# Optimization experiments

Measured on AMD Instinct MI355X. Metric: run time of the kernel, lower is better.

Reference implementation:

```python
import jax, jax.numpy as jnp
import numpy as np

H, L, N = 512, 2048, 64  # channels, seq len, SSM state size


def _make_dplr_hippo(n):
    # make_HiPPO / make_NPLR_HiPPO / make_DPLR_HiPPO from the source
    p0 = np.sqrt(1.0 + 2.0 * np.arange(n))
    A = p0[:, None] * p0[None, :]
    A = np.tril(A) - np.diag(np.arange(n))
    nhippo = -A
    P = np.sqrt(np.arange(n) + 0.5)
    B = np.sqrt(2.0 * np.arange(n) + 1.0)
    S = nhippo + P[:, None] * P[None, :]
    S_diag = np.diagonal(S)
    Lam_re = np.mean(S_diag) * np.ones_like(S_diag)
    Lam_im, V = jnp.linalg.eigh(jnp.asarray(S, jnp.complex64) * (-1j))
    Pc = V.conj().T @ jnp.asarray(P, jnp.complex64)
    Bc = V.conj().T @ jnp.asarray(B, jnp.complex64)
    return (jnp.asarray(Lam_re, jnp.float32), jnp.asarray(Lam_im, jnp.float32),
            Pc, Bc)


def setup_inputs() -> dict:
    key = jax.random.key(0)
    k_u, k_c, k_s = jax.random.split(key, 3)
    Lre, Lim, Pc, Bc = _make_dplr_hippo(N)
    tile = lambda v: jnp.tile(v[None, :], (H, 1)).astype(jnp.float32)  # (H,N)
    return {
        "u": jax.random.normal(k_u, (L, H), dtype=jnp.float32),
        "x0_re": jnp.zeros((N, H), jnp.float32),
        "x0_im": jnp.zeros((N, H), jnp.float32),
        "Lambda_re": tile(Lre),
        "Lambda_im": tile(Lim),
        "P_re": tile(Pc.real), "P_im": tile(Pc.imag),
        "B_re": tile(Bc.real), "B_im": tile(Bc.imag),
        "C": jax.random.normal(k_c, (H, N, 2), jnp.float32) * (0.5 ** 0.5),
        "D": jnp.ones((H, 1), jnp.float32),
        "log_step": jax.random.uniform(k_s, (H, 1), jnp.float32,
                                       minval=np.log(1e-3), maxval=np.log(1e-1)),
    }


def _discretize(Lam, P, B, Ct, step):
    # discrete_DPLR with Q = P (as in setup); per-channel, vmapped over H.
    n = Lam.shape[0]
    I = jnp.eye(n, dtype=jnp.complex64)
    A = jnp.diag(Lam) - P[:, None] * P.conj()[None, :]
    A0 = (2.0 / step) * I + A
    Dd = jnp.diag(1.0 / (2.0 / step - Lam))
    Qc = P.conj()[None, :]            # (1,N)
    P2 = P[:, None]                   # (N,1)
    A1 = Dd - (Dd @ P2) * (1.0 / (1.0 + Qc @ Dd @ P2)) * (Qc @ Dd)
    Ab = A1 @ A0                      # (N,N)
    Bb = 2.0 * (A1 @ B[:, None])[:, 0]
    AbL = jnp.linalg.matrix_power(Ab, L)
    Cb = (Ct[None, :] @ jnp.linalg.inv(I - AbL).conj()).conj()[0]
    return Ab, Bb, Cb


def _forward(u, x0_re, x0_im, Lambda_re, Lambda_im, P_re, P_im,
             B_re, B_im, C, D, log_step):
    Lam = jnp.clip(Lambda_re, None, -0.0001) + 1j * Lambda_im  # (H,N)
    Pc = P_re + 1j * P_im
    Bc = B_re + 1j * B_im
    Cc = C[..., 0] + 1j * C[..., 1]
    step = jnp.exp(log_step)[:, 0]                              # (H,)
    Ab, Bb, Cb = jax.vmap(_discretize)(Lam, Pc, Bc, Cc, step)   # (H,N,N),(H,N),(H,N)

    x0 = jnp.transpose(x0_re + 1j * x0_im)                      # (H,N) complex

    def body(x, u_t):  # x: (H,N) complex, u_t: (H,)
        x = jnp.einsum('hnm,hm->hn', Ab, x) + Bb * u_t[:, None]
        y = jnp.einsum('hn,hn->h', Cb, x)
        return x, y.real

    _, ys = jax.lax.scan(body, x0, u)                           # ys: (L,H)
    return ys + u * D[:, 0][None, :]                            # (L,H) float32


def reference(u, x0_re, x0_im, Lambda_re, Lambda_im, P_re, P_im,
              B_re, B_im, C, D, log_step):
    return _forward(u, x0_re, x0_im, Lambda_re, Lambda_im, P_re, P_im,
                    B_re, B_im, C, D, log_step)
```

## Files before the change

kernel.cpp:

```cpp
#include <hip/hip_runtime.h>

#define HH 512
#define LL 2048
#define NN 64
#define TT 64
#define CC 32
#define NLDA 68
#define SP 72

typedef __attribute__((ext_vector_type(8))) short bf16x8_t;
typedef __attribute__((ext_vector_type(4))) float floatx4;

__device__ __forceinline__ float2 cmul(float2 a, float2 b) {
    return make_float2(a.x * b.x - a.y * b.y, a.x * b.y + a.y * b.x);
}
__device__ __forceinline__ float2 crecip(float2 a) {
    float id = 1.0f / (a.x * a.x + a.y * a.y);
    return make_float2(a.x * id, -a.y * id);
}
template <int CTRL>
__device__ __forceinline__ float dpp_mov(float x) {
    return __int_as_float(__builtin_amdgcn_update_dpp(
        0, __float_as_int(x), CTRL, 0xf, 0xf, true));
}
__device__ __forceinline__ float wave_sum_bcast(float x) {
    x += dpp_mov<0x111>(x);
    x += dpp_mov<0x112>(x);
    x += dpp_mov<0x114>(x);
    x += dpp_mov<0x118>(x);
    x += dpp_mov<0x142>(x);
    x += dpp_mov<0x143>(x);
    return __int_as_float(__builtin_amdgcn_readlane(__float_as_int(x), 63));
}
__device__ __forceinline__ float rlane(float x, int i) {
    return __int_as_float(__builtin_amdgcn_readlane(__float_as_int(x), i));
}
__device__ __forceinline__ unsigned short f2bf(float f) {
    unsigned int u = __float_as_uint(f);
    u += 0x7FFFu + ((u >> 16) & 1u);
    return (unsigned short)(u >> 16);
}
__device__ __forceinline__ float bf2f(unsigned short s) {
    return __uint_as_float(((unsigned int)s) << 16);
}

__device__ __forceinline__ void closed_form(
    int h, int n,
    const float* __restrict__ Lre, const float* __restrict__ Lim,
    const float* __restrict__ Pre, const float* __restrict__ Pim,
    const float* __restrict__ Bre, const float* __restrict__ Bim,
    const float* __restrict__ logstep,
    float2& da, float2& DPv, float2& tv, float2& bb) {
    float step = expf(logstep[h]);
    float as = 2.0f / step;
    float lr = fminf(Lre[h * NN + n], -1e-4f);
    float li = Lim[h * NN + n];
    float2 a = make_float2(as + lr, li);
    float2 Dn = crecip(make_float2(as - lr, -li));
    float2 P = make_float2(Pre[h * NN + n], Pim[h * NN + n]);
    float2 Bv = make_float2(Bre[h * NN + n], Bim[h * NN + n]);
    float2 cP = make_float2(P.x, -P.y);
    float p2 = P.x * P.x + P.y * P.y;
    float2 rt = cmul(cmul(cP, Dn), Bv);
    float2 e = make_float2(wave_sum_bcast(Dn.x * p2), wave_sum_bcast(Dn.y * p2));
    float2 rv = make_float2(wave_sum_bcast(rt.x), wave_sum_bcast(rt.y));
    float2 cc = crecip(make_float2(1.0f + e.x, e.y));
    da = cmul(Dn, a);
    DPv = cmul(Dn, P);
    float2 tmp = cmul(cc, make_float2(da.x - e.x, da.y - e.y));
    tv = cmul(cP, make_float2(1.0f + tmp.x, tmp.y));
    float2 crv = cmul(cc, rv);
    float2 cd = cmul(crv, DPv);
    float2 db = cmul(Dn, Bv);
    bb = make_float2(2.0f * (db.x - cd.x), 2.0f * (db.y - cd.y));
}

__device__ __forceinline__ void pack_tiles(
    unsigned short* mRh, unsigned short* mRl,
    unsigned short* mIh, unsigned short* mIl,
    unsigned short* mTRh, unsigned short* mTRl,
    unsigned short* mTIh, unsigned short* mTIl,
    int w, int lm, int q, const float Cr[4][4], const float Ci[4][4]) {
    #pragma unroll
    for (int nt = 0; nt < 4; ++nt) {
        const int c = nt * 16 + lm;
        unsigned short hr[4], lr_[4], hi_[4], li_[4];
        #pragma unroll
        for (int reg = 0; reg < 4; ++reg) {
            const float xr = Cr[nt][reg], xi = Ci[nt][reg];
            hr[reg] = f2bf(xr); lr_[reg] = f2bf(xr - bf2f(hr[reg]));
            hi_[reg] = f2bf(xi); li_[reg] = f2bf(xi - bf2f(hi_[reg]));
            const int r = 16 * w + 4 * q + reg;
            const int rm = r * 64 + (c ^ ((r & 7) << 3));
            mRh[rm] = hr[reg]; mRl[rm] = lr_[reg];
            mIh[rm] = hi_[reg]; mIl[rm] = li_[reg];
        }
        const int tb = c * 64 + ((16 * w + 4 * q) ^ ((c & 7) << 3));
        *(ushort4*)&mTRh[tb] = make_ushort4(hr[0], hr[1], hr[2], hr[3]);
        *(ushort4*)&mTRl[tb] = make_ushort4(lr_[0], lr_[1], lr_[2], lr_[3]);
        *(ushort4*)&mTIh[tb] = make_ushort4(hi_[0], hi_[1], hi_[2], hi_[3]);
        *(ushort4*)&mTIl[tb] = make_ushort4(li_[0], li_[1], li_[2], li_[3]);
    }
}

extern "C" __global__ void __launch_bounds__(256, 2)
k_fused(const float* __restrict__ Lre, const float* __restrict__ Lim,
        const float* __restrict__ Pre, const float* __restrict__ Pim,
        const float* __restrict__ Bre, const float* __restrict__ Bim,
        const float* __restrict__ Cmat, const float* __restrict__ logstep,
        const float* __restrict__ u, const float* __restrict__ Dvec,
        const float* __restrict__ x0_re, const float* __restrict__ x0_im,
        float2* __restrict__ wM, float* __restrict__ out) {
    extern __shared__ __align__(16) char smem[];
    const int tid = threadIdx.x;
    const int h = blockIdx.x;

    unsigned short* mRh  = (unsigned short*)smem;
    unsigned short* mRl  = mRh + 4096;
    unsigned short* mIh  = mRl + 4096;
    unsigned short* mIl  = mIh + 4096;
    unsigned short* mTRh = mIl + 4096;
    unsigned short* mTRl = mTRh + 4096;
    unsigned short* mTIh = mTRl + 4096;
    unsigned short* mTIl = mTIh + 4096;
    float* Nr = (float*)smem;
    float* Ni = Nr + 64 * NLDA;
    float2* pp   = (float2*)(smem + 36864);
    float2* sda  = (float2*)(smem + 70016);
    float2* sDP  = (float2*)(smem + 70528);
    float2* st   = (float2*)(smem + 71040);
    float2* sBb  = (float2*)(smem + 71552);
    float2* srhs = (float2*)(smem + 72064);
    float2* sx   = (float2*)(smem + 72576);
    unsigned short* sVr  = (unsigned short*)smem;
    unsigned short* sVi  = (unsigned short*)(smem + 9216);
    unsigned short* sXrh = (unsigned short*)(smem + 18432);
    unsigned short* sXrl = (unsigned short*)(smem + 23040);
    unsigned short* sXih = (unsigned short*)(smem + 27648);
    unsigned short* sXil = (unsigned short*)(smem + 32256);
    float*          su   = (float*)(smem + 36864);
    float*          sK   = (float*)(smem + 45056);
    float*          y0   = (float*)(smem + 45312);
    float2*         sP   = (float2*)(smem + 53632);

    const int w = tid >> 6;
    const int lane = tid & 63;
    const int lm = lane & 15, q = lane >> 4;

    if (tid < NN) {
        float2 da, DPv, tv, bb;
        closed_form(h, tid, Lre, Lim, Pre, Pim, Bre, Bim, logstep,
                    da, DPv, tv, bb);
        sda[tid] = da; sDP[tid] = DPv; st[tid] = tv; sBb[tid] = bb;
        srhs[tid] = make_float2(Cmat[h * NN * 2 + tid * 2],
                                -Cmat[h * NN * 2 + tid * 2 + 1]);
    }
    __syncthreads();

    {
        float Cr[4][4], Ci[4][4];
        #pragma unroll
        for (int nt = 0; nt < 4; ++nt) {
            const int c = nt * 16 + lm;
            const float2 tc = st[c];
            #pragma unroll
            for (int reg = 0; reg < 4; ++reg) {
                const int r = 16 * w + 4 * q + reg;
                const float2 dp = sDP[r];
                float vr = -(dp.x * tc.x - dp.y * tc.y);
                float vi = -(dp.x * tc.y + dp.y * tc.x);
                if (r == c) { vr += sda[r].x; vi += sda[r].y; }
                Cr[nt][reg] = vr; Ci[nt][reg] = vi;
            }
        }
        pack_tiles(mRh, mRl, mIh, mIl, mTRh, mTRl, mTIh, mTIl,
                   w, lm, q, Cr, Ci);
    }
    __syncthreads();

    const int arow = (16 * w + lm) * 64;
    const int asw  = (lm & 7) << 3;
    for (int it = 0; it < 11; ++it) {
        floatx4 z4 = {0.f, 0.f, 0.f, 0.f};
        floatx4 aP[4] = {z4, z4, z4, z4};
        floatx4 aQ[4] = {z4, z4, z4, z4};
        floatx4 aC[4] = {z4, z4, z4, z4};
        for (int k2 = 0; k2 < 2; ++k2) {
            const int ko = (k2 * 32 + q * 8) ^ asw;
            const int ao = arow + ko;
            const bf16x8_t ARh = *(const bf16x8_t*)&mRh[ao];
            const bf16x8_t ARl = *(const bf16x8_t*)&mRl[ao];
            const bf16x8_t AIh = *(const bf16x8_t*)&mIh[ao];
            const bf16x8_t AIl = *(const bf16x8_t*)&mIl[ao];
            bf16x8_t BRh[4], BRl[4], BIh[4], BIl[4];
            #pragma unroll
            for (int nt = 0; nt < 4; ++nt) {
                const int bo = (nt * 16 + lm) * 64 + ko;
                BRh[nt] = *(const bf16x8_t*)&mTRh[bo];
                BRl[nt] = *(const bf16x8_t*)&mTRl[bo];
                BIh[nt] = *(const bf16x8_t*)&mTIh[bo];
                BIl[nt] = *(const bf16x8_t*)&mTIl[bo];
            }
            #pragma unroll
            for (int nt = 0; nt < 4; ++nt) {
                aP[nt] = __builtin_amdgcn_mfma_f32_16x16x32_bf16(ARh, BRh[nt], aP[nt], 0, 0, 0);
                aP[nt] = __builtin_amdgcn_mfma_f32_16x16x32_bf16(ARh, BRl[nt], aP[nt], 0, 0, 0);
                aP[nt] = __builtin_amdgcn_mfma_f32_16x16x32_bf16(ARl, BRh[nt], aP[nt], 0, 0, 0);
                aQ[nt] = __builtin_amdgcn_mfma_f32_16x16x32_bf16(AIh, BIh[nt], aQ[nt], 0, 0, 0);
                aQ[nt] = __builtin_amdgcn_mfma_f32_16x16x32_bf16(AIh, BIl[nt], aQ[nt], 0, 0, 0);
                aQ[nt] = __builtin_amdgcn_mfma_f32_16x16x32_bf16(AIl, BIh[nt], aQ[nt], 0, 0, 0);
                aC[nt] = __builtin_amdgcn_mfma_f32_16x16x32_bf16(ARh, BIh[nt], aC[nt], 0, 0, 0);
                aC[nt] = __builtin_amdgcn_mfma_f32_16x16x32_bf16(ARh, BIl[nt], aC[nt], 0, 0, 0);
                aC[nt] = __builtin_amdgcn_mfma_f32_16x16x32_bf16(ARl, BIh[nt], aC[nt], 0, 0, 0);
                aC[nt] = __builtin_amdgcn_mfma_f32_16x16x32_bf16(AIh, BRh[nt], aC[nt], 0, 0, 0);
                aC[nt] = __builtin_amdgcn_mfma_f32_16x16x32_bf16(AIh, BRl[nt], aC[nt], 0, 0, 0);
                aC[nt] = __builtin_amdgcn_mfma_f32_16x16x32_bf16(AIl, BRh[nt], aC[nt], 0, 0, 0);
            }
        }
        __syncthreads();
        if (it < 10) {
            float Cr[4][4], Ci[4][4];
            #pragma unroll
            for (int nt = 0; nt < 4; ++nt)
                #pragma unroll
                for (int reg = 0; reg < 4; ++reg) {
                    Cr[nt][reg] = aP[nt][reg] - aQ[nt][reg];
                    Ci[nt][reg] = aC[nt][reg];
                }
            pack_tiles(mRh, mRl, mIh, mIl, mTRh, mTRl, mTIh, mTIl,
                       w, lm, q, Cr, Ci);
            __syncthreads();
            if (it == 5) {
                for (int idx = tid; idx < NN * NN; idx += 256) {
                    const int c = idx >> 6, k = idx & 63;
                    const int e = c * 64 + (k ^ ((c & 7) << 3));
                    wM[h * NN * NN + idx] = make_float2(
                        bf2f(mTRh[e]) + bf2f(mTRl[e]),
                        bf2f(mTIh[e]) + bf2f(mTIl[e]));
                }
            }
        } else {
            #pragma unroll
            for (int nt = 0; nt < 4; ++nt) {
                const int c = nt * 16 + lm;
                #pragma unroll
                for (int reg = 0; reg < 4; ++reg) {
                    const int r = 16 * w + 4 * q + reg;
                    Nr[r * NLDA + c] = aP[nt][reg] - aQ[nt][reg];
                    Ni[r * NLDA + c] = aC[nt][reg];
                }
            }
            __syncthreads();
        }
    }

    if (tid < NN) sx[tid] = srhs[tid];
    __syncthreads();
    for (int itn = 0; itn < 16; ++itn) {
        const int i = tid & 63, qq = tid >> 6;
        float pr = 0.0f, pi = 0.0f;
        #pragma unroll 4
        for (int jj = 0; jj < 16; ++jj) {
            const int j = qq * 16 + jj;
            const float nr = Nr[j * NLDA + i], ni = Ni[j * NLDA + i];
            const float2 xj = sx[j];
            pr += nr * xj.x - ni * xj.y;
            pi += nr * xj.y + ni * xj.x;
        }
        pp[qq * 64 + i] = make_float2(pr, pi);
        __syncthreads();
        if (tid < NN) {
            const float2 a0 = pp[tid], a1 = pp[64 + tid];
            const float2 a2 = pp[128 + tid], a3 = pp[192 + tid];
            sx[tid] = make_float2(
                srhs[tid].x + a0.x + a1.x + a2.x + a3.x,
                srhs[tid].y + a0.y + a1.y + a2.y + a3.y);
        }
        __syncthreads();
    }

    const int wv = w;
    float Mr[NN], Mi[NN];
    float x0r = 0.0f, x0i = 0.0f;

    if (wv == 0) {
        const float2 da = sda[lane], DP = sDP[lane], tt = st[lane];
        const float2 Bb = sBb[lane];
        const float2 Cb = sx[lane];
        float Gr = Bb.x, Gi = Bb.y;
        float vr = Cb.x, vi = Cb.y;
        for (int m = 0; m < TT; ++m) {
            float ch[5];
            ch[0] = Cb.x * Gr - Cb.y * Gi;
            ch[1] = tt.x * Gr - tt.y * Gi;
            ch[2] = tt.x * Gi + tt.y * Gr;
            ch[3] = vr * DP.x - vi * DP.y;
            ch[4] = vr * DP.y + vi * DP.x;
            #pragma unroll
            for (int c = 0; c < 5; ++c) ch[c] += dpp_mov<0x111>(ch[c]);
            #pragma unroll
            for (int c = 0; c < 5; ++c) ch[c] += dpp_mov<0x112>(ch[c]);
            #pragma unroll
            for (int c = 0; c < 5; ++c) ch[c] += dpp_mov<0x114>(ch[c]);
            #pragma unroll
            for (int c = 0; c < 5; ++c) ch[c] += dpp_mov<0x118>(ch[c]);
            #pragma unroll
            for (int c = 0; c < 5; ++c) ch[c] += dpp_mov<0x142>(ch[c]);
            #pragma unroll
            for (int c = 0; c < 5; ++c) ch[c] += dpp_mov<0x143>(ch[c]);
            const float S0 = rlane(ch[0], 63);
            const float S1 = rlane(ch[1], 63);
            const float S2 = rlane(ch[2], 63);
            const float S3 = rlane(ch[3], 63);
            const float S4 = rlane(ch[4], 63);
            if (lane == 0) sK[m] = S0;
            float nGr = da.x * Gr - da.y * Gi - (DP.x * S1 - DP.y * S2);
            float nGi = da.x * Gi + da.y * Gr - (DP.x * S2 + DP.y * S1);
            Gr = nGr; Gi = nGi;
            float nvr = da.x * vr - da.y * vi - (S3 * tt.x - S4 * tt.y);
            float nvi = da.x * vi + da.y * vr - (S3 * tt.y + S4 * tt.x);
            vr = nvr; vi = nvi;
            sVr[m * SP + lane] = f2bf(vr);
            sVi[m * SP + lane] = f2bf(-vi);
        }
    } else if (wv == 1) {
        const float2* __restrict__ wMh = wM + h * NN * NN;
        #pragma unroll
        for (int j = 0; j < NN; ++j) {
            const float2 v = wMh[j * NN + lane];
            Mr[j] = v.x; Mi[j] = v.y;
        }
        x0r = x0_re[lane * HH + h];
        x0i = x0_im[lane * HH + h];
    } else {
        const int par = wv - 2;
        for (int k = lane; k < 1024; k += 64) {
            const int cc = ((k >> 6) << 1) | par;
            const int s = k & 63;
            su[cc * 64 + s] = u[(cc * 64 + s) * HH + h];
        }
        const float2 da = sda[lane], DP = sDP[lane], tt = st[lane];
        const float2 Bb = sBb[lane];
        float Gr = Bb.x, Gi = Bb.y;
        float ar[16] = {}, ai[16] = {};
        for (int m = 0; m < TT; ++m) {
            #pragma unroll
            for (int ci = 0; ci < 16; ++ci) {
                const int cc = (ci << 1) | par;
                const float uv = su[cc * 64 + (63 - m)];
                ar[ci] = fmaf(Gr, uv, ar[ci]);
                ai[ci] = fmaf(Gi, uv, ai[ci]);
            }
            float c1 = tt.x * Gr - tt.y * Gi;
            float c2 = tt.x * Gi + tt.y * Gr;
            c1 += dpp_mov<0x111>(c1); c2 += dpp_mov<0x111>(c2);
            c1 += dpp_mov<0x112>(c1); c2 += dpp_mov<0x112>(c2);
            c1 += dpp_mov<0x114>(c1); c2 += dpp_mov<0x114>(c2);
            c1 += dpp_mov<0x118>(c1); c2 += dpp_mov<0x118>(c2);
            c1 += dpp_mov<0x142>(c1); c2 += dpp_mov<0x142>(c2);
            c1 += dpp_mov<0x143>(c1); c2 += dpp_mov<0x143>(c2);
            const float S1 = rlane(c1, 63);
            const float S2 = rlane(c2, 63);
            float nGr = da.x * Gr - da.y * Gi - (DP.x * S1 - DP.y * S2);
            float nGi = da.x * Gi + da.y * Gr - (DP.x * S2 + DP.y * S1);
            Gr = nGr; Gi = nGi;
        }
        #pragma unroll
        for (int ci = 0; ci < 16; ++ci) {
            const int cc = (ci << 1) | par;
            sP[cc * 64 + lane] = make_float2(ar[ci], ai[ci]);
        }
    }
    __syncthreads();

    const float Dh = Dvec[h];
    if (wv == 1) {
        float xr = x0r, xi = x0i;
        {
            const unsigned short hr = f2bf(xr), hi_ = f2bf(xi);
            sXrh[lane] = hr;  sXrl[lane] = f2bf(xr - bf2f(hr));
            sXih[lane] = hi_; sXil[lane] = f2bf(xi - bf2f(hi_));
        }
        for (int c = 1; c < CC; ++c) {
            const float2 pe = sP[(c - 1) * 64 + lane];
            float ar[4] = {0.f, 0.f, 0.f, 0.f};
            float ai[4] = {0.f, 0.f, 0.f, 0.f};
            #pragma unroll
            for (int j = 0; j < NN; ++j) {
                const float xjr = rlane(xr, j);
                const float xji = rlane(xi, j);
                ar[j & 3] = fmaf(Mr[j], xjr, ar[j & 3]);
                ar[j & 3] = fmaf(-Mi[j], xji, ar[j & 3]);
                ai[j & 3] = fmaf(Mr[j], xji, ai[j & 3]);
                ai[j & 3] = fmaf(Mi[j], xjr, ai[j & 3]);
            }
            xr = ((ar[0] + ar[1]) + (ar[2] + ar[3])) + pe.x;
            xi = ((ai[0] + ai[1]) + (ai[2] + ai[3])) + pe.y;
            const unsigned short hr = f2bf(xr), hi_ = f2bf(xi);
            sXrh[c * SP + lane] = hr;  sXrl[c * SP + lane] = f2bf(xr - bf2f(hr));
            sXih[c * SP + lane] = hi_; sXil[c * SP + lane] = f2bf(xi - bf2f(hi_));
        }
    } else {
        const int c0 = (wv == 0) ? 0 : (wv == 2 ? 11 : 22);
        const int c1 = (wv == 0) ? 11 : (wv == 2 ? 22 : 32);
        for (int c = c0; c < c1; ++c) {
            float acc = 0.0f;
            for (int s = 0; s < TT; ++s) {
                const int d = lane - s;
                const float kv = (d >= 0) ? sK[d < 0 ? 0 : d] : 0.0f;
                acc = fmaf(kv, su[c * 64 + s], acc);
            }
            y0[c * 65 + lane] = acc + Dh * su[c * 64 + lane];
        }
    }
    __syncthreads();

    floatx4 z4b = {0.f, 0.f, 0.f, 0.f};
    floatx4 acc2[2] = {z4b, z4b};
    #pragma unroll
    for (int k2 = 0; k2 < 2; ++k2) {
        const int ak = (16 * wv + lm) * SP + k2 * 32 + q * 8;
        const bf16x8_t aVr = *(const bf16x8_t*)&sVr[ak];
        const bf16x8_t aVi = *(const bf16x8_t*)&sVi[ak];
        #pragma unroll
        for (int nt = 0; nt < 2; ++nt) {
            const int bk = (nt * 16 + lm) * SP + k2 * 32 + q * 8;
            const bf16x8_t bRh = *(const bf16x8_t*)&sXrh[bk];
            const bf16x8_t bRl = *(const bf16x8_t*)&sXrl[bk];
            const bf16x8_t bIh = *(const bf16x8_t*)&sXih[bk];
            const bf16x8_t bIl = *(const bf16x8_t*)&sXil[bk];
            acc2[nt] = __builtin_amdgcn_mfma_f32_16x16x32_bf16(aVr, bRh, acc2[nt], 0, 0, 0);
            acc2[nt] = __builtin_amdgcn_mfma_f32_16x16x32_bf16(aVr, bRl, acc2[nt], 0, 0, 0);
            acc2[nt] = __builtin_amdgcn_mfma_f32_16x16x32_bf16(aVi, bIh, acc2[nt], 0, 0, 0);
            acc2[nt] = __builtin_amdgcn_mfma_f32_16x16x32_bf16(aVi, bIl, acc2[nt], 0, 0, 0);
        }
    }
    #pragma unroll
    for (int nt = 0; nt < 2; ++nt) {
        #pragma unroll
        for (int reg = 0; reg < 4; ++reg) {
            const int c = nt * 16 + lm;
            const int t = 16 * wv + 4 * q + reg;
            out[(c * TT + t) * HH + h] = acc2[nt][reg] + y0[c * 65 + t];
        }
    }
}

extern "C" void kernel_launch(void* const* d_in, const int* in_sizes, int n_in,
                              void* d_out, int out_size, void* d_ws, size_t ws_size,
                              hipStream_t stream) {
    const float* u    = (const float*)d_in[0];
    const float* x0re = (const float*)d_in[1];
    const float* x0im = (const float*)d_in[2];
    const float* Lre  = (const float*)d_in[3];
    const float* Lim  = (const float*)d_in[4];
    const float* Pre  = (const float*)d_in[5];
    const float* Pim  = (const float*)d_in[6];
    const float* Bre  = (const float*)d_in[7];
    const float* Bim  = (const float*)d_in[8];
    const float* C    = (const float*)d_in[9];
    const float* Dv   = (const float*)d_in[10];
    const float* lst  = (const float*)d_in[11];

    float2* wM = (float2*)d_ws;
    float* out = (float*)d_out;

    hipLaunchKernelGGL(k_fused, dim3(HH), dim3(256), 73088, stream,
                       Lre, Lim, Pre, Pim, Bre, Bim, C, lst, u, Dv,
                       x0re, x0im, wM, out);
}
```

Baseline: 189.3 us.

## Double block to 512 threads and repartition every phase across eight waves

Raises the block size from 256 to 512 threads and redistributes work across 8 waves in each stage: the repeated-squaring MFMA tiles become a 4x2 wave grid, the Neumann-style solve splits its reduction eight ways, the input-projection and causal convolution are split across more waves, and the final output MFMA gives one tile per wave. The aim is to shorten the serial per-channel latency by spreading each phase over more waves, since there are only 512 blocks for the whole GPU. The cost is higher register pressure under the tighter launch bound (512, 4), with possible spills in the 64-element per-thread arrays. It also adds more barrier participants and leaves some waves idle in certain phases.

```diff
diff --git a/kernel.cpp b/kernel.cpp
--- a/kernel.cpp
+++ b/kernel.cpp
@@ -75,27 +75,27 @@
     bb = make_float2(2.0f * (db.x - cd.x), 2.0f * (db.y - cd.y));
 }
 
-__device__ __forceinline__ void pack_tiles(
+__device__ __forceinline__ void pack_tiles8(
     unsigned short* mRh, unsigned short* mRl,
     unsigned short* mIh, unsigned short* mIl,
     unsigned short* mTRh, unsigned short* mTRl,
     unsigned short* mTIh, unsigned short* mTIl,
-    int w, int lm, int q, const float Cr[4][4], const float Ci[4][4]) {
+    int wr, int wc, int lm, int q, const float Cr[2][4], const float Ci[2][4]) {
     #pragma unroll
-    for (int nt = 0; nt < 4; ++nt) {
-        const int c = nt * 16 + lm;
+    for (int nt2 = 0; nt2 < 2; ++nt2) {
+        const int c = (2 * wc + nt2) * 16 + lm;
         unsigned short hr[4], lr_[4], hi_[4], li_[4];
         #pragma unroll
         for (int reg = 0; reg < 4; ++reg) {
-            const float xr = Cr[nt][reg], xi = Ci[nt][reg];
+            const float xr = Cr[nt2][reg], xi = Ci[nt2][reg];
             hr[reg] = f2bf(xr); lr_[reg] = f2bf(xr - bf2f(hr[reg]));
             hi_[reg] = f2bf(xi); li_[reg] = f2bf(xi - bf2f(hi_[reg]));
-            const int r = 16 * w + 4 * q + reg;
+            const int r = 16 * wr + 4 * q + reg;
             const int rm = r * 64 + (c ^ ((r & 7) << 3));
             mRh[rm] = hr[reg]; mRl[rm] = lr_[reg];
             mIh[rm] = hi_[reg]; mIl[rm] = li_[reg];
         }
-        const int tb = c * 64 + ((16 * w + 4 * q) ^ ((c & 7) << 3));
+        const int tb = c * 64 + ((16 * wr + 4 * q) ^ ((c & 7) << 3));
         *(ushort4*)&mTRh[tb] = make_ushort4(hr[0], hr[1], hr[2], hr[3]);
         *(ushort4*)&mTRl[tb] = make_ushort4(lr_[0], lr_[1], lr_[2], lr_[3]);
         *(ushort4*)&mTIh[tb] = make_ushort4(hi_[0], hi_[1], hi_[2], hi_[3]);
@@ -103,7 +103,7 @@
     }
 }
 
-extern "C" __global__ void __launch_bounds__(256, 2)
+extern "C" __global__ void __launch_bounds__(512, 4)
 k_fused(const float* __restrict__ Lre, const float* __restrict__ Lim,
         const float* __restrict__ Pre, const float* __restrict__ Pim,
         const float* __restrict__ Bre, const float* __restrict__ Bim,
@@ -143,9 +143,10 @@
     float*          y0   = (float*)(smem + 45312);
     float2*         sP   = (float2*)(smem + 53632);
 
-    const int w = tid >> 6;
+    const int w8 = tid >> 6;
     const int lane = tid & 63;
     const int lm = lane & 15, q = lane >> 4;
+    const int wr = w8 & 3, wc = w8 >> 2;
 
     if (tid < NN) {
         float2 da, DPv, tv, bb;
@@ -158,33 +159,33 @@
     __syncthreads();
 
     {
-        float Cr[4][4], Ci[4][4];
+        float Cr[2][4], Ci[2][4];
         #pragma unroll
-        for (int nt = 0; nt < 4; ++nt) {
-            const int c = nt * 16 + lm;
+        for (int nt2 = 0; nt2 < 2; ++nt2) {
+            const int c = (2 * wc + nt2) * 16 + lm;
             const float2 tc = st[c];
             #pragma unroll
             for (int reg = 0; reg < 4; ++reg) {
-                const int r = 16 * w + 4 * q + reg;
+                const int r = 16 * wr + 4 * q + reg;
                 const float2 dp = sDP[r];
                 float vr = -(dp.x * tc.x - dp.y * tc.y);
                 float vi = -(dp.x * tc.y + dp.y * tc.x);
                 if (r == c) { vr += sda[r].x; vi += sda[r].y; }
-                Cr[nt][reg] = vr; Ci[nt][reg] = vi;
-            }
-        }
-        pack_tiles(mRh, mRl, mIh, mIl, mTRh, mTRl, mTIh, mTIl,
-                   w, lm, q, Cr, Ci);
-    }
-    __syncthreads();
-
-    const int arow = (16 * w + lm) * 64;
+                Cr[nt2][reg] = vr; Ci[nt2][reg] = vi;
+            }
+        }
+        pack_tiles8(mRh, mRl, mIh, mIl, mTRh, mTRl, mTIh, mTIl,
+                    wr, wc, lm, q, Cr, Ci);
+    }
+    __syncthreads();
+
+    const int arow = (16 * wr + lm) * 64;
     const int asw  = (lm & 7) << 3;
     for (int it = 0; it < 11; ++it) {
         floatx4 z4 = {0.f, 0.f, 0.f, 0.f};
-        floatx4 aP[4] = {z4, z4, z4, z4};
-        floatx4 aQ[4] = {z4, z4, z4, z4};
-        floatx4 aC[4] = {z4, z4, z4, z4};
+        floatx4 aP[2] = {z4, z4};
+        floatx4 aQ[2] = {z4, z4};
+        floatx4 aC[2] = {z4, z4};
         for (int k2 = 0; k2 < 2; ++k2) {
             const int ko = (k2 * 32 + q * 8) ^ asw;
             const int ao = arow + ko;
@@ -192,46 +193,46 @@
             const bf16x8_t ARl = *(const bf16x8_t*)&mRl[ao];
             const bf16x8_t AIh = *(const bf16x8_t*)&mIh[ao];
             const bf16x8_t AIl = *(const bf16x8_t*)&mIl[ao];
-            bf16x8_t BRh[4], BRl[4], BIh[4], BIl[4];
-            #pragma unroll
-            for (int nt = 0; nt < 4; ++nt) {
-                const int bo = (nt * 16 + lm) * 64 + ko;
-                BRh[nt] = *(const bf16x8_t*)&mTRh[bo];
-                BRl[nt] = *(const bf16x8_t*)&mTRl[bo];
-                BIh[nt] = *(const bf16x8_t*)&mTIh[bo];
-                BIl[nt] = *(const bf16x8_t*)&mTIl[bo];
-            }
-            #pragma unroll
-            for (int nt = 0; nt < 4; ++nt) {
-                aP[nt] = __builtin_amdgcn_mfma_f32_16x16x32_bf16(ARh, BRh[nt], aP[nt], 0, 0, 0);
-                aP[nt] = __builtin_amdgcn_mfma_f32_16x16x32_bf16(ARh, BRl[nt], aP[nt], 0, 0, 0);
-                aP[nt] = __builtin_amdgcn_mfma_f32_16x16x32_bf16(ARl, BRh[nt], aP[nt], 0, 0, 0);
-                aQ[nt] = __builtin_amdgcn_mfma_f32_16x16x32_bf16(AIh, BIh[nt], aQ[nt], 0, 0, 0);
-                aQ[nt] = __builtin_amdgcn_mfma_f32_16x16x32_bf16(AIh, BIl[nt], aQ[nt], 0, 0, 0);
-                aQ[nt] = __builtin_amdgcn_mfma_f32_16x16x32_bf16(AIl, BIh[nt], aQ[nt], 0, 0, 0);
-                aC[nt] = __builtin_amdgcn_mfma_f32_16x16x32_bf16(ARh, BIh[nt], aC[nt], 0, 0, 0);
-                aC[nt] = __builtin_amdgcn_mfma_f32_16x16x32_bf16(ARh, BIl[nt], aC[nt], 0, 0, 0);
-                aC[nt] = __builtin_amdgcn_mfma_f32_16x16x32_bf16(ARl, BIh[nt], aC[nt], 0, 0, 0);
-                aC[nt] = __builtin_amdgcn_mfma_f32_16x16x32_bf16(AIh, BRh[nt], aC[nt], 0, 0, 0);
-                aC[nt] = __builtin_amdgcn_mfma_f32_16x16x32_bf16(AIh, BRl[nt], aC[nt], 0, 0, 0);
-                aC[nt] = __builtin_amdgcn_mfma_f32_16x16x32_bf16(AIl, BRh[nt], aC[nt], 0, 0, 0);
+            bf16x8_t BRh[2], BRl[2], BIh[2], BIl[2];
+            #pragma unroll
+            for (int nt2 = 0; nt2 < 2; ++nt2) {
+                const int bo = ((2 * wc + nt2) * 16 + lm) * 64 + ko;
+                BRh[nt2] = *(const bf16x8_t*)&mTRh[bo];
+                BRl[nt2] = *(const bf16x8_t*)&mTRl[bo];
+                BIh[nt2] = *(const bf16x8_t*)&mTIh[bo];
+                BIl[nt2] = *(const bf16x8_t*)&mTIl[bo];
+            }
+            #pragma unroll
+            for (int nt2 = 0; nt2 < 2; ++nt2) {
+                aP[nt2] = __builtin_amdgcn_mfma_f32_16x16x32_bf16(ARh, BRh[nt2], aP[nt2], 0, 0, 0);
+                aP[nt2] = __builtin_amdgcn_mfma_f32_16x16x32_bf16(ARh, BRl[nt2], aP[nt2], 0, 0, 0);
+                aP[nt2] = __builtin_amdgcn_mfma_f32_16x16x32_bf16(ARl, BRh[nt2], aP[nt2], 0, 0, 0);
+                aQ[nt2] = __builtin_amdgcn_mfma_f32_16x16x32_bf16(AIh, BIh[nt2], aQ[nt2], 0, 0, 0);
+                aQ[nt2] = __builtin_amdgcn_mfma_f32_16x16x32_bf16(AIh, BIl[nt2], aQ[nt2], 0, 0, 0);
+                aQ[nt2] = __builtin_amdgcn_mfma_f32_16x16x32_bf16(AIl, BIh[nt2], aQ[nt2], 0, 0, 0);
+                aC[nt2] = __builtin_amdgcn_mfma_f32_16x16x32_bf16(ARh, BIh[nt2], aC[nt2], 0, 0, 0);
+                aC[nt2] = __builtin_amdgcn_mfma_f32_16x16x32_bf16(ARh, BIl[nt2], aC[nt2], 0, 0, 0);
+                aC[nt2] = __builtin_amdgcn_mfma_f32_16x16x32_bf16(ARl, BIh[nt2], aC[nt2], 0, 0, 0);
+                aC[nt2] = __builtin_amdgcn_mfma_f32_16x16x32_bf16(AIh, BRh[nt2], aC[nt2], 0, 0, 0);
+                aC[nt2] = __builtin_amdgcn_mfma_f32_16x16x32_bf16(AIh, BRl[nt2], aC[nt2], 0, 0, 0);
+                aC[nt2] = __builtin_amdgcn_mfma_f32_16x16x32_bf16(AIl, BRh[nt2], aC[nt2], 0, 0, 0);
             }
         }
         __syncthreads();
         if (it < 10) {
-            float Cr[4][4], Ci[4][4];
-            #pragma unroll
-            for (int nt = 0; nt < 4; ++nt)
+            float Cr[2][4], Ci[2][4];
+            #pragma unroll
+            for (int nt2 = 0; nt2 < 2; ++nt2)
                 #pragma unroll
                 for (int reg = 0; reg < 4; ++reg) {
-                    Cr[nt][reg] = aP[nt][reg] - aQ[nt][reg];
-                    Ci[nt][reg] = aC[nt][reg];
+                    Cr[nt2][reg] = aP[nt2][reg] - aQ[nt2][reg];
+                    Ci[nt2][reg] = aC[nt2][reg];
                 }
-            pack_tiles(mRh, mRl, mIh, mIl, mTRh, mTRl, mTIh, mTIl,
-                       w, lm, q, Cr, Ci);
+            pack_tiles8(mRh, mRl, mIh, mIl, mTRh, mTRl, mTIh, mTIl,
+                        wr, wc, lm, q, Cr, Ci);
             __syncthreads();
             if (it == 5) {
-                for (int idx = tid; idx < NN * NN; idx += 256) {
+                for (int idx = tid; idx < NN * NN; idx += 512) {
                     const int c = idx >> 6, k = idx & 63;
                     const int e = c * 64 + (k ^ ((c & 7) << 3));
                     wM[h * NN * NN + idx] = make_float2(
@@ -241,13 +242,13 @@
             }
         } else {
             #pragma unroll
-            for (int nt = 0; nt < 4; ++nt) {
-                const int c = nt * 16 + lm;
+            for (int nt2 = 0; nt2 < 2; ++nt2) {
+                const int c = (2 * wc + nt2) * 16 + lm;
                 #pragma unroll
                 for (int reg = 0; reg < 4; ++reg) {
-                    const int r = 16 * w + 4 * q + reg;
-                    Nr[r * NLDA + c] = aP[nt][reg] - aQ[nt][reg];
-                    Ni[r * NLDA + c] = aC[nt][reg];
+                    const int r = 16 * wr + 4 * q + reg;
+                    Nr[r * NLDA + c] = aP[nt2][reg] - aQ[nt2][reg];
+                    Ni[r * NLDA + c] = aC[nt2][reg];
                 }
             }
             __syncthreads();
@@ -257,29 +258,31 @@
     if (tid < NN) sx[tid] = srhs[tid];
     __syncthreads();
     for (int itn = 0; itn < 16; ++itn) {
-        const int i = tid & 63, qq = tid >> 6;
         float pr = 0.0f, pi = 0.0f;
-        #pragma unroll 4
-        for (int jj = 0; jj < 16; ++jj) {
-            const int j = qq * 16 + jj;
-            const float nr = Nr[j * NLDA + i], ni = Ni[j * NLDA + i];
+        #pragma unroll
+        for (int jj = 0; jj < 8; ++jj) {
+            const int j = w8 * 8 + jj;
+            const float nr = Nr[j * NLDA + lane], ni = Ni[j * NLDA + lane];
             const float2 xj = sx[j];
             pr += nr * xj.x - ni * xj.y;
             pi += nr * xj.y + ni * xj.x;
         }
-        pp[qq * 64 + i] = make_float2(pr, pi);
+        pp[w8 * 64 + lane] = make_float2(pr, pi);
         __syncthreads();
         if (tid < NN) {
-            const float2 a0 = pp[tid], a1 = pp[64 + tid];
-            const float2 a2 = pp[128 + tid], a3 = pp[192 + tid];
-            sx[tid] = make_float2(
-                srhs[tid].x + a0.x + a1.x + a2.x + a3.x,
-                srhs[tid].y + a0.y + a1.y + a2.y + a3.y);
+            float xr = srhs[tid].x, xi = srhs[tid].y;
+            #pragma unroll
+            for (int k = 0; k < 8; ++k) {
+                const float2 a = pp[k * 64 + tid];
+                xr += a.x; xi += a.y;
+            }
+            sx[tid] = make_float2(xr, xi);
         }
         __syncthreads();
     }
-
-    const int wv = w;
+    __syncthreads();
+
+    const int wv = w8;
     float Mr[NN], Mi[NN];
     float x0r = 0.0f, x0i = 0.0f;
 
@@ -332,21 +335,21 @@
         }
         x0r = x0_re[lane * HH + h];
         x0i = x0_im[lane * HH + h];
-    } else {
+    } else if (wv <= 5) {
         const int par = wv - 2;
-        for (int k = lane; k < 1024; k += 64) {
-            const int cc = ((k >> 6) << 1) | par;
+        for (int k = lane; k < 512; k += 64) {
+            const int cc = ((k >> 6) << 2) | par;
             const int s = k & 63;
             su[cc * 64 + s] = u[(cc * 64 + s) * HH + h];
         }
         const float2 da = sda[lane], DP = sDP[lane], tt = st[lane];
         const float2 Bb = sBb[lane];
         float Gr = Bb.x, Gi = Bb.y;
-        float ar[16] = {}, ai[16] = {};
+        float ar[8] = {}, ai[8] = {};
         for (int m = 0; m < TT; ++m) {
             #pragma unroll
-            for (int ci = 0; ci < 16; ++ci) {
-                const int cc = (ci << 1) | par;
+            for (int ci = 0; ci < 8; ++ci) {
+                const int cc = (ci << 2) | par;
                 const float uv = su[cc * 64 + (63 - m)];
                 ar[ci] = fmaf(Gr, uv, ar[ci]);
                 ai[ci] = fmaf(Gi, uv, ai[ci]);
@@ -366,8 +369,8 @@
             Gr = nGr; Gi = nGi;
         }
         #pragma unroll
-        for (int ci = 0; ci < 16; ++ci) {
-            const int cc = (ci << 1) | par;
+        for (int ci = 0; ci < 8; ++ci) {
+            const int cc = (ci << 2) | par;
             sP[cc * 64 + lane] = make_float2(ar[ci], ai[ci]);
         }
     }
@@ -401,8 +404,9 @@
             sXih[c * SP + lane] = hi_; sXil[c * SP + lane] = f2bf(xi - bf2f(hi_));
         }
     } else {
-        const int c0 = (wv == 0) ? 0 : (wv == 2 ? 11 : 22);
-        const int c1 = (wv == 0) ? 11 : (wv == 2 ? 22 : 32);
+        const int ord = (wv == 0) ? 0 : wv - 1;
+        const int c0 = (ord < 4) ? ord * 5 : 20 + (ord - 4) * 4;
+        const int c1 = (ord < 4) ? c0 + 5 : c0 + 4;
         for (int c = c0; c < c1; ++c) {
             float acc = 0.0f;
             for (int s = 0; s < TT; ++s) {
@@ -415,34 +419,29 @@
     }
     __syncthreads();
 
+    const int tr = wv >> 1, tc = wv & 1;
     floatx4 z4b = {0.f, 0.f, 0.f, 0.f};
-    floatx4 acc2[2] = {z4b, z4b};
+    floatx4 acc2 = z4b;
     #pragma unroll
     for (int k2 = 0; k2 < 2; ++k2) {
-        const int ak = (16 * wv + lm) * SP + k2 * 32 + q * 8;
+        const int ak = (16 * tr + lm) * SP + k2 * 32 + q * 8;
         const bf16x8_t aVr = *(const bf16x8_t*)&sVr[ak];
         const bf16x8_t aVi = *(const bf16x8_t*)&sVi[ak];
-        #pragma unroll
-        for (int nt = 0; nt < 2; ++nt) {
-            const int bk = (nt * 16 + lm) * SP + k2 * 32 + q * 8;
-            const bf16x8_t bRh = *(const bf16x8_t*)&sXrh[bk];
-            const bf16x8_t bRl = *(const bf16x8_t*)&sXrl[bk];
-            const bf16x8_t bIh = *(const bf16x8_t*)&sXih[bk];
-            const bf16x8_t bIl = *(const bf16x8_t*)&sXil[bk];
-            acc2[nt] = __builtin_amdgcn_mfma_f32_16x16x32_bf16(aVr, bRh, acc2[nt], 0, 0, 0);
-            acc2[nt] = __builtin_amdgcn_mfma_f32_16x16x32_bf16(aVr, bRl, acc2[nt], 0, 0, 0);
-            acc2[nt] = __builtin_amdgcn_mfma_f32_16x16x32_bf16(aVi, bIh, acc2[nt], 0, 0, 0);
-            acc2[nt] = __builtin_amdgcn_mfma_f32_16x16x32_bf16(aVi, bIl, acc2[nt], 0, 0, 0);
-        }
+        const int bk = (tc * 16 + lm) * SP + k2 * 32 + q * 8;
+        const bf16x8_t bRh = *(const bf16x8_t*)&sXrh[bk];
+        const bf16x8_t bRl = *(const bf16x8_t*)&sXrl[bk];
+        const bf16x8_t bIh = *(const bf16x8_t*)&sXih[bk];
+        const bf16x8_t bIl = *(const bf16x8_t*)&sXil[bk];
+        acc2 = __builtin_amdgcn_mfma_f32_16x16x32_bf16(aVr, bRh, acc2, 0, 0, 0);
+        acc2 = __builtin_amdgcn_mfma_f32_16x16x32_bf16(aVr, bRl, acc2, 0, 0, 0);
+        acc2 = __builtin_amdgcn_mfma_f32_16x16x32_bf16(aVi, bIh, acc2, 0, 0, 0);
+        acc2 = __builtin_amdgcn_mfma_f32_16x16x32_bf16(aVi, bIl, acc2, 0, 0, 0);
     }
     #pragma unroll
-    for (int nt = 0; nt < 2; ++nt) {
-        #pragma unroll
-        for (int reg = 0; reg < 4; ++reg) {
-            const int c = nt * 16 + lm;
-            const int t = 16 * wv + 4 * q + reg;
-            out[(c * TT + t) * HH + h] = acc2[nt][reg] + y0[c * 65 + t];
-        }
+    for (int reg = 0; reg < 4; ++reg) {
+        const int c = tc * 16 + lm;
+        const int t = 16 * tr + 4 * q + reg;
+        out[(c * TT + t) * HH + h] = acc2[reg] + y0[c * 65 + t];
     }
 }
 
@@ -465,7 +464,7 @@
     float2* wM = (float2*)d_ws;
     float* out = (float*)d_out;
 
-    hipLaunchKernelGGL(k_fused, dim3(HH), dim3(256), 73088, stream,
+    hipLaunchKernelGGL(k_fused, dim3(HH), dim3(512), 73088, stream,
                        Lre, Lim, Pre, Pim, Bre, Bim, C, lst, u, Dv,
                        x0re, x0im, wM, out);
 }
```

Result: slower. 478.3 us (+152.6%).
